# Kernel tuning notes

Hardware: AMD Instinct MI355X
Metric: run time of the kernel (lower is better)

The kernel has to match this reference:

```python
import jax, jax.numpy as jnp
import numpy as np

N_FEATURE = 12
SIGMA = 0.015
NODES = jnp.linspace(0.0, 0.3, 12)  # RBF centers, matches torch.linspace(0,0.3,12)

B, N, K, FIN = 16, 4096, 32, 4


def setup_inputs() -> dict:
    key = jax.random.key(0)
    ks = jax.random.split(key, 24)

    def make_d(ki, kd):
        idx = jax.random.randint(ki, (B, N, K), 0, N).astype(jnp.float32)
        dist = jax.random.uniform(kd, (B, N, K), minval=0.0, maxval=0.3)
        return jnp.stack([idx, dist], axis=-1)  # [B,N,K,2]

    def lin(kw, kb, fin, fout):
        W = jax.random.normal(kw, (fin, fout), jnp.float32) * (1.0 / np.sqrt(fin))
        b = jax.random.normal(kb, (fout,), jnp.float32) * 0.01
        return W, b

    x = jax.random.normal(ks[0], (B, N, FIN), jnp.float32)
    d1 = make_d(ks[1], ks[2])
    d0 = make_d(ks[3], ks[4])
    dm1 = make_d(ks[5], ks[6])
    mask = jnp.ones((B, N), dtype=bool)

    We, be = lin(ks[7], ks[8], FIN, N_FEATURE)
    Wm1, bm1 = lin(ks[9], ks[10], N_FEATURE + 12, N_FEATURE)
    Wu1, bu1 = lin(ks[11], ks[12], 2 * N_FEATURE, N_FEATURE)
    Wm0, bm0 = lin(ks[13], ks[14], N_FEATURE + 12, N_FEATURE)
    Wu0, bu0 = lin(ks[15], ks[16], 2 * N_FEATURE, N_FEATURE)
    Wmm1, bmm1 = lin(ks[17], ks[18], N_FEATURE + 12, N_FEATURE)
    Wum1, bum1 = lin(ks[19], ks[20], 2 * N_FEATURE, N_FEATURE)

    return {"x": x, "d1": d1, "d0": d0, "dm1": dm1, "mask": mask,
            "We": We, "be": be, "Wm1": Wm1, "bm1": bm1, "Wu1": Wu1, "bu1": bu1,
            "Wm0": Wm0, "bm0": bm0, "Wu0": Wu0, "bu0": bu0,
            "Wmm1": Wmm1, "bmm1": bmm1, "Wum1": Wum1, "bum1": bum1}


def _branch(h, d, Wm, bm, Wu, bu):
    # d: [B,N,K,2] -> channel 0 neighbor index, channel 1 distance
    idx = d[..., 0].astype(jnp.int32)                     # [B,N,K]
    rbf = jnp.exp(-((d[..., 1][..., None] - NODES) ** 2) / (2.0 * SIGMA ** 2))  # [B,N,K,12]
    hj = jax.vmap(lambda hb, ib: hb[ib])(h, idx)          # gather: [B,N,K,F]
    hd = jnp.concatenate([hj, rbf], axis=-1)              # [B,N,K,F+12]
    m = jax.nn.relu(hd @ Wm + bm).sum(axis=2)             # [B,N,F]
    return jax.nn.sigmoid(jnp.concatenate([h, m], axis=-1) @ Wu + bu)  # [B,N,F]


def reference(x, d1, d0, dm1, mask,
              We, be, Wm1, bm1, Wu1, bu1,
              Wm0, bm0, Wu0, bu0,
              Wmm1, bmm1, Wum1, bum1):
    h = jax.nn.relu(x @ We + be)                          # [B,N,12]
    h1 = _branch(h, d1, Wm1, bm1, Wu1, bu1)
    h0 = _branch(h, d0, Wm0, bm0, Wu0, bu0)
    hm1 = _branch(h, dm1, Wmm1, bmm1, Wum1, bum1)
    return (h1, h0, hm1)
```

## Files before the change

kernel.cpp:

```cpp
#include <hip/hip_runtime.h>
#include <hip/hip_fp16.h>
#include <math.h>

#define BBAT 16
#define NNODE 4096
#define KNB 32
#define NF 12
#define TBL 512
#define TMAIN 1024
#define NPB 256

#define LDS_BYTES 122880

__device__ __forceinline__ __half2 u2h(unsigned int u) { __half2 h; __builtin_memcpy(&h, &u, 4); return h; }
__device__ __forceinline__ unsigned int h2u(__half2 h) { unsigned int u; __builtin_memcpy(&u, &h, 4); return u; }

__device__ __forceinline__ void phi_entry(int e, const float* __restrict__ Wm, float* ph)
{
    float dd = (float)e * (0.3f / (float)TBL);
    float rbf[12];
#pragma unroll
    for (int j = 0; j < 12; j++) {
        float t = dd - (0.3f / 11.0f) * (float)j;
        rbf[j] = expf(-2222.2222222222f * t * t);
    }
#pragma unroll
    for (int c = 0; c < NF; c++) {
        float s = 0.0f;
#pragma unroll
        for (int j = 0; j < 12; j++) s = fmaf(rbf[j], Wm[(12 + j) * NF + c], s);
        ph[c] = s;
    }
}

__global__ __launch_bounds__(256) void prep_kernel(
    const float* __restrict__ x, const float* __restrict__ We, const float* __restrict__ be,
    const float* __restrict__ Wm1, const float* __restrict__ bm1,
    const float* __restrict__ Wm0, const float* __restrict__ bm0,
    const float* __restrict__ Wmm1, const float* __restrict__ bmm1,
    uint2* __restrict__ gS0, uint2* __restrict__ gS1, uint2* __restrict__ gS2,
    uint2* __restrict__ T01, uint2* __restrict__ T23, uint2* __restrict__ T45,
    uint2* __restrict__ D01, uint2* __restrict__ D23, uint2* __restrict__ D45)
{
    const int node = blockIdx.x * 256 + threadIdx.x;
    float4 xv = ((const float4*)x)[node];
    float hv[NF];
#pragma unroll
    for (int f = 0; f < NF; f++) {
        float s = be[f];
        s = fmaf(xv.x, We[0 * NF + f], s);
        s = fmaf(xv.y, We[1 * NF + f], s);
        s = fmaf(xv.z, We[2 * NF + f], s);
        s = fmaf(xv.w, We[3 * NF + f], s);
        hv[f] = fmaxf(s, 0.0f);
    }

#define DO_G(BR, WM, BM) {                                                     \
        float g[NF];                                                           \
        _Pragma("unroll") for (int c = 0; c < NF; c++) {                       \
            float s = BM[c];                                                   \
            _Pragma("unroll") for (int j = 0; j < NF; j++)                     \
                s = fmaf(hv[j], WM[j * NF + c], s);                            \
            g[c] = s;                                                          \
        }                                                                      \
        const size_t o = (size_t)(BR) * 65536 + node;                          \
        gS0[o] = make_uint2(h2u(__floats2half2_rn(g[0], g[1])),                \
                            h2u(__floats2half2_rn(g[2], g[3])));               \
        gS1[o] = make_uint2(h2u(__floats2half2_rn(g[4], g[5])),                \
                            h2u(__floats2half2_rn(g[6], g[7])));               \
        gS2[o] = make_uint2(h2u(__floats2half2_rn(g[8], g[9])),                \
                            h2u(__floats2half2_rn(g[10], g[11])));             \
    }
    DO_G(0, Wm1, bm1)
    DO_G(1, Wm0, bm0)
    DO_G(2, Wmm1, bmm1)
#undef DO_G

    if (blockIdx.x < 3) {
        const int br = blockIdx.x;
        const float* Wm = (br == 0) ? Wm1 : (br == 1) ? Wm0 : Wmm1;
        for (int i = threadIdx.x; i < TBL; i += 256) {
            float p0[NF], p1[NF];
            phi_entry(i, Wm, p0);
            phi_entry(i + 1, Wm, p1);
            __half2 w0 = __floats2half2_rn(p0[0],  p0[1]);
            __half2 w1 = __floats2half2_rn(p0[2],  p0[3]);
            __half2 w2 = __floats2half2_rn(p0[4],  p0[5]);
            __half2 w3 = __floats2half2_rn(p0[6],  p0[7]);
            __half2 w4 = __floats2half2_rn(p0[8],  p0[9]);
            __half2 w5 = __floats2half2_rn(p0[10], p0[11]);
            __half2 v0 = __floats2half2_rn(p1[0],  p1[1]);
            __half2 v1 = __floats2half2_rn(p1[2],  p1[3]);
            __half2 v2 = __floats2half2_rn(p1[4],  p1[5]);
            __half2 v3 = __floats2half2_rn(p1[6],  p1[7]);
            __half2 v4 = __floats2half2_rn(p1[8],  p1[9]);
            __half2 v5 = __floats2half2_rn(p1[10], p1[11]);
            const int o = br * TBL + i;
            T01[o] = make_uint2(h2u(w0), h2u(w1));
            T23[o] = make_uint2(h2u(w2), h2u(w3));
            T45[o] = make_uint2(h2u(w4), h2u(w5));
            D01[o] = make_uint2(h2u(__hsub2(v0, w0)), h2u(__hsub2(v1, w1)));
            D23[o] = make_uint2(h2u(__hsub2(v2, w2)), h2u(__hsub2(v3, w3)));
            D45[o] = make_uint2(h2u(__hsub2(v4, w4)), h2u(__hsub2(v5, w5)));
        }
    }
}

__global__ __launch_bounds__(TMAIN) void main_kernel(
    const float* __restrict__ x, const float* __restrict__ We, const float* __restrict__ be,
    const uint2* __restrict__ gS0, const uint2* __restrict__ gS1, const uint2* __restrict__ gS2,
    const uint2* __restrict__ T01, const uint2* __restrict__ T23, const uint2* __restrict__ T45,
    const uint2* __restrict__ D01, const uint2* __restrict__ D23, const uint2* __restrict__ D45,
    const float* __restrict__ d1, const float* __restrict__ d0, const float* __restrict__ dm1,
    const float* __restrict__ Wu1, const float* __restrict__ bu1,
    const float* __restrict__ Wu0, const float* __restrict__ bu0,
    const float* __restrict__ Wum1, const float* __restrict__ bum1,
    float* __restrict__ out)
{
    extern __shared__ char smem[];
    uint2* G0l  = (uint2*)smem;
    uint2* G1l  = (uint2*)(smem + 32768);
    uint2* G2l  = (uint2*)(smem + 65536);
    uint2* T01l = (uint2*)(smem + 98304);
    uint2* T23l = (uint2*)(smem + 102400);
    uint2* T45l = (uint2*)(smem + 106496);
    uint2* D01l = (uint2*)(smem + 110592);
    uint2* D23l = (uint2*)(smem + 114688);
    uint2* D45l = (uint2*)(smem + 118784);

    const int w = blockIdx.x;
    const int xcd = w & 7;
    const int k = w >> 3;
    const int slice = xcd + 8 * (k >> 4);
    const int chunk = k & 15;
    const int br = slice / BBAT;
    const int b  = slice % BBAT;

    const int tid = threadIdx.x;
    const int nl = tid >> 2, sub = tid & 3;
    const int n = chunk * NPB + nl;

    const float* dsel = (br == 0) ? d1 : (br == 1) ? d0 : dm1;

    const float4* dp = (const float4*)(dsel + ((size_t)b * NNODE + n) * (size_t)(KNB * 2)) + sub * 4;
    float4 dr0 = dp[0], dr1 = dp[1], dr2 = dp[2], dr3 = dp[3];

    {
        const uint4* s0 = (const uint4*)(gS0 + (size_t)slice * NNODE);
        const uint4* s1 = (const uint4*)(gS1 + (size_t)slice * NNODE);
        const uint4* s2 = (const uint4*)(gS2 + (size_t)slice * NNODE);
        uint4* L0 = (uint4*)G0l; uint4* L1 = (uint4*)G1l; uint4* L2 = (uint4*)G2l;
#pragma unroll
        for (int it = 0; it < 2; it++) {
            const int i = it * TMAIN + tid;
            L0[i] = s0[i];
            L1[i] = s1[i];
            L2[i] = s2[i];
        }
        if (tid < TBL) {
            const int o = br * TBL + tid;
            T01l[tid] = T01[o];
            T23l[tid] = T23[o];
            T45l[tid] = T45[o];
            D01l[tid] = D01[o];
            D23l[tid] = D23[o];
            D45l[tid] = D45[o];
        }
    }
    __syncthreads();

    int   jv[8];
    float uv[8];
    jv[0] = (int)dr0.x; uv[0] = dr0.y * ((float)TBL / 0.3f);
    jv[1] = (int)dr0.z; uv[1] = dr0.w * ((float)TBL / 0.3f);
    jv[2] = (int)dr1.x; uv[2] = dr1.y * ((float)TBL / 0.3f);
    jv[3] = (int)dr1.z; uv[3] = dr1.w * ((float)TBL / 0.3f);
    jv[4] = (int)dr2.x; uv[4] = dr2.y * ((float)TBL / 0.3f);
    jv[5] = (int)dr2.z; uv[5] = dr2.w * ((float)TBL / 0.3f);
    jv[6] = (int)dr3.x; uv[6] = dr3.y * ((float)TBL / 0.3f);
    jv[7] = (int)dr3.z; uv[7] = dr3.w * ((float)TBL / 0.3f);

    float m[NF];
#pragma unroll
    for (int f = 0; f < NF; f++) m[f] = 0.0f;

#define ACC(O, G, T0, DT) {                                                    \
        __half2 phi = __hfma2(f2, u2h(DT), u2h(T0));                           \
        __half2 s2 = __hadd2(u2h(G), phi);                                     \
        float2 sf = __half22float2(s2);                                        \
        m[O]     += fmaxf(sf.x, 0.0f);                                         \
        m[O + 1] += fmaxf(sf.y, 0.0f);                                         \
    }

#define EDGE(GC0, GC1, GC2, GN0, GN1, GN2, E, PREF)                            \
    {                                                                          \
        if (PREF) { int jn = jv[(E) + 1];                                      \
            GN0 = G0l[jn]; GN1 = G1l[jn]; GN2 = G2l[jn]; }                     \
        float uu = uv[E];                                                      \
        int ii = (int)uu;                                                      \
        ii = min(ii, TBL - 1);                                                 \
        float fr = uu - (float)ii;                                             \
        __half2 f2 = __float2half2_rn(fr);                                     \
        uint2 ta = T01l[ii], tb = T23l[ii], tc = T45l[ii];                     \
        uint2 da = D01l[ii], db = D23l[ii], dc = D45l[ii];                     \
        ACC(0,  GC0.x, ta.x, da.x)                                             \
        ACC(2,  GC0.y, ta.y, da.y)                                             \
        ACC(4,  GC1.x, tb.x, db.x)                                             \
        ACC(6,  GC1.y, tb.y, db.y)                                             \
        ACC(8,  GC2.x, tc.x, dc.x)                                             \
        ACC(10, GC2.y, tc.y, dc.y)                                             \
    }

    uint2 pa0, pa1, pa2, pb0, pb1, pb2;
    { int j0 = jv[0]; pa0 = G0l[j0]; pa1 = G1l[j0]; pa2 = G2l[j0]; }
    EDGE(pa0, pa1, pa2, pb0, pb1, pb2, 0, 1)
    EDGE(pb0, pb1, pb2, pa0, pa1, pa2, 1, 1)
    EDGE(pa0, pa1, pa2, pb0, pb1, pb2, 2, 1)
    EDGE(pb0, pb1, pb2, pa0, pa1, pa2, 3, 1)
    EDGE(pa0, pa1, pa2, pb0, pb1, pb2, 4, 1)
    EDGE(pb0, pb1, pb2, pa0, pa1, pa2, 5, 1)
    EDGE(pa0, pa1, pa2, pb0, pb1, pb2, 6, 1)
    EDGE(pb0, pb1, pb2, pa0, pa1, pa2, 7, 0)

#undef EDGE
#undef ACC

#pragma unroll
    for (int f = 0; f < NF; f++) m[f] += __shfl_xor(m[f], 1);
#pragma unroll
    for (int f = 0; f < NF; f++) m[f] += __shfl_xor(m[f], 2);

    const float* Wu = (br == 0) ? Wu1 : (br == 1) ? Wu0 : Wum1;
    const float* bu = (br == 0) ? bu1 : (br == 1) ? bu0 : bum1;

    float4 xv = ((const float4*)x)[(size_t)b * NNODE + n];
    float hv[NF];
#pragma unroll
    for (int f = 0; f < NF; f++) {
        float s = be[f];
        s = fmaf(xv.x, We[0 * NF + f], s);
        s = fmaf(xv.y, We[1 * NF + f], s);
        s = fmaf(xv.z, We[2 * NF + f], s);
        s = fmaf(xv.w, We[3 * NF + f], s);
        hv[f] = fmaxf(s, 0.0f);
    }

    const int f0 = sub * 3;
    float* op = out + ((size_t)slice * NNODE + n) * NF + f0;
#pragma unroll
    for (int ff = 0; ff < 3; ff++) {
        const int f = f0 + ff;
        float a = bu[f];
#pragma unroll
        for (int j = 0; j < NF; j++) a = fmaf(hv[j], Wu[j * NF + f], a);
#pragma unroll
        for (int j = 0; j < NF; j++) a = fmaf(m[j], Wu[(NF + j) * NF + f], a);
        op[ff] = 1.0f / (1.0f + __expf(-a));
    }
}

extern "C" void kernel_launch(void* const* d_in, const int* in_sizes, int n_in,
                              void* d_out, int out_size, void* d_ws, size_t ws_size,
                              hipStream_t stream)
{
    const float* x    = (const float*)d_in[0];
    const float* d1   = (const float*)d_in[1];
    const float* d0   = (const float*)d_in[2];
    const float* dm1  = (const float*)d_in[3];
    const float* We   = (const float*)d_in[5];
    const float* be   = (const float*)d_in[6];
    const float* Wm1  = (const float*)d_in[7];
    const float* bm1  = (const float*)d_in[8];
    const float* Wu1  = (const float*)d_in[9];
    const float* bu1  = (const float*)d_in[10];
    const float* Wm0  = (const float*)d_in[11];
    const float* bm0  = (const float*)d_in[12];
    const float* Wu0  = (const float*)d_in[13];
    const float* bu0  = (const float*)d_in[14];
    const float* Wmm1 = (const float*)d_in[15];
    const float* bmm1 = (const float*)d_in[16];
    const float* Wum1 = (const float*)d_in[17];
    const float* bum1 = (const float*)d_in[18];

    char* ws = (char*)d_ws;
    uint2* gS0 = (uint2*)ws;
    uint2* gS1 = (uint2*)(ws + 1572864);
    uint2* gS2 = (uint2*)(ws + 3145728);
    uint2* T01 = (uint2*)(ws + 4718592);
    uint2* T23 = (uint2*)(ws + 4730880);
    uint2* T45 = (uint2*)(ws + 4743168);
    uint2* D01 = (uint2*)(ws + 4755456);
    uint2* D23 = (uint2*)(ws + 4767744);
    uint2* D45 = (uint2*)(ws + 4780032);

    hipFuncSetAttribute((const void*)main_kernel,
                        hipFuncAttributeMaxDynamicSharedMemorySize, LDS_BYTES);

    prep_kernel<<<dim3(256), 256, 0, stream>>>(
        x, We, be, Wm1, bm1, Wm0, bm0, Wmm1, bmm1,
        gS0, gS1, gS2, T01, T23, T45, D01, D23, D45);
    main_kernel<<<dim3(768), TMAIN, LDS_BYTES, stream>>>(
        x, We, be, gS0, gS1, gS2, T01, T23, T45, D01, D23, D45,
        d1, d0, dm1, Wu1, bu1, Wu0, bu0, Wum1, bum1, (float*)d_out);
}
```

Before: 152.5 us.

## Pack gather and table arrays into wider LDS records and batch edge loads

```diff
diff --git a/kernel.cpp b/kernel.cpp
--- a/kernel.cpp
+++ b/kernel.cpp
@@ -38,9 +38,8 @@
     const float* __restrict__ Wm1, const float* __restrict__ bm1,
     const float* __restrict__ Wm0, const float* __restrict__ bm0,
     const float* __restrict__ Wmm1, const float* __restrict__ bmm1,
-    uint2* __restrict__ gS0, uint2* __restrict__ gS1, uint2* __restrict__ gS2,
-    uint2* __restrict__ T01, uint2* __restrict__ T23, uint2* __restrict__ T45,
-    uint2* __restrict__ D01, uint2* __restrict__ D23, uint2* __restrict__ D45)
+    uint4* __restrict__ gA, uint2* __restrict__ gB,
+    uint4* __restrict__ TA, uint4* __restrict__ TB, uint4* __restrict__ TC)
 {
     const int node = blockIdx.x * 256 + threadIdx.x;
     float4 xv = ((const float4*)x)[node];
@@ -64,12 +63,12 @@
             g[c] = s;                                                          \
         }                                                                      \
         const size_t o = (size_t)(BR) * 65536 + node;                          \
-        gS0[o] = make_uint2(h2u(__floats2half2_rn(g[0], g[1])),                \
-                            h2u(__floats2half2_rn(g[2], g[3])));               \
-        gS1[o] = make_uint2(h2u(__floats2half2_rn(g[4], g[5])),                \
-                            h2u(__floats2half2_rn(g[6], g[7])));               \
-        gS2[o] = make_uint2(h2u(__floats2half2_rn(g[8], g[9])),                \
-                            h2u(__floats2half2_rn(g[10], g[11])));             \
+        gA[o] = make_uint4(h2u(__floats2half2_rn(g[0], g[1])),                 \
+                           h2u(__floats2half2_rn(g[2], g[3])),                 \
+                           h2u(__floats2half2_rn(g[4], g[5])),                 \
+                           h2u(__floats2half2_rn(g[6], g[7])));                \
+        gB[o] = make_uint2(h2u(__floats2half2_rn(g[8], g[9])),                 \
+                           h2u(__floats2half2_rn(g[10], g[11])));              \
     }
     DO_G(0, Wm1, bm1)
     DO_G(1, Wm0, bm0)
@@ -96,21 +95,17 @@
             __half2 v4 = __floats2half2_rn(p1[8],  p1[9]);
             __half2 v5 = __floats2half2_rn(p1[10], p1[11]);
             const int o = br * TBL + i;
-            T01[o] = make_uint2(h2u(w0), h2u(w1));
-            T23[o] = make_uint2(h2u(w2), h2u(w3));
-            T45[o] = make_uint2(h2u(w4), h2u(w5));
-            D01[o] = make_uint2(h2u(__hsub2(v0, w0)), h2u(__hsub2(v1, w1)));
-            D23[o] = make_uint2(h2u(__hsub2(v2, w2)), h2u(__hsub2(v3, w3)));
-            D45[o] = make_uint2(h2u(__hsub2(v4, w4)), h2u(__hsub2(v5, w5)));
+            TA[o] = make_uint4(h2u(w0), h2u(w1), h2u(__hsub2(v0, w0)), h2u(__hsub2(v1, w1)));
+            TB[o] = make_uint4(h2u(w2), h2u(w3), h2u(__hsub2(v2, w2)), h2u(__hsub2(v3, w3)));
+            TC[o] = make_uint4(h2u(w4), h2u(w5), h2u(__hsub2(v4, w4)), h2u(__hsub2(v5, w5)));
         }
     }
 }
 
-__global__ __launch_bounds__(TMAIN) void main_kernel(
+__global__ __launch_bounds__(TMAIN, 4) void main_kernel(
     const float* __restrict__ x, const float* __restrict__ We, const float* __restrict__ be,
-    const uint2* __restrict__ gS0, const uint2* __restrict__ gS1, const uint2* __restrict__ gS2,
-    const uint2* __restrict__ T01, const uint2* __restrict__ T23, const uint2* __restrict__ T45,
-    const uint2* __restrict__ D01, const uint2* __restrict__ D23, const uint2* __restrict__ D45,
+    const uint4* __restrict__ gA, const uint2* __restrict__ gB,
+    const uint4* __restrict__ TA, const uint4* __restrict__ TB, const uint4* __restrict__ TC,
     const float* __restrict__ d1, const float* __restrict__ d0, const float* __restrict__ dm1,
     const float* __restrict__ Wu1, const float* __restrict__ bu1,
     const float* __restrict__ Wu0, const float* __restrict__ bu0,
@@ -118,15 +113,11 @@
     float* __restrict__ out)
 {
     extern __shared__ char smem[];
-    uint2* G0l  = (uint2*)smem;
-    uint2* G1l  = (uint2*)(smem + 32768);
-    uint2* G2l  = (uint2*)(smem + 65536);
-    uint2* T01l = (uint2*)(smem + 98304);
-    uint2* T23l = (uint2*)(smem + 102400);
-    uint2* T45l = (uint2*)(smem + 106496);
-    uint2* D01l = (uint2*)(smem + 110592);
-    uint2* D23l = (uint2*)(smem + 114688);
-    uint2* D45l = (uint2*)(smem + 118784);
+    uint4* GAl = (uint4*)smem;
+    uint2* GBl = (uint2*)(smem + 65536);
+    uint4* TAl = (uint4*)(smem + 98304);
+    uint4* TBl = (uint4*)(smem + 106496);
+    uint4* TCl = (uint4*)(smem + 114688);
 
     const int w = blockIdx.x;
     const int xcd = w & 7;
@@ -146,39 +137,42 @@
     float4 dr0 = dp[0], dr1 = dp[1], dr2 = dp[2], dr3 = dp[3];
 
     {
-        const uint4* s0 = (const uint4*)(gS0 + (size_t)slice * NNODE);
-        const uint4* s1 = (const uint4*)(gS1 + (size_t)slice * NNODE);
-        const uint4* s2 = (const uint4*)(gS2 + (size_t)slice * NNODE);
-        uint4* L0 = (uint4*)G0l; uint4* L1 = (uint4*)G1l; uint4* L2 = (uint4*)G2l;
-#pragma unroll
-        for (int it = 0; it < 2; it++) {
-            const int i = it * TMAIN + tid;
-            L0[i] = s0[i];
-            L1[i] = s1[i];
-            L2[i] = s2[i];
-        }
+        const uint4* sA = gA + (size_t)slice * NNODE;
+        const uint4* sB = (const uint4*)(gB + (size_t)slice * NNODE);
+        uint4* LB = (uint4*)GBl;
+#pragma unroll
+        for (int it = 0; it < 4; it++) GAl[it * TMAIN + tid] = sA[it * TMAIN + tid];
+#pragma unroll
+        for (int it = 0; it < 2; it++) LB[it * TMAIN + tid] = sB[it * TMAIN + tid];
         if (tid < TBL) {
             const int o = br * TBL + tid;
-            T01l[tid] = T01[o];
-            T23l[tid] = T23[o];
-            T45l[tid] = T45[o];
-            D01l[tid] = D01[o];
-            D23l[tid] = D23[o];
-            D45l[tid] = D45[o];
+            TAl[tid] = TA[o];
+            TBl[tid] = TB[o];
+            TCl[tid] = TC[o];
         }
     }
     __syncthreads();
 
-    int   jv[8];
-    float uv[8];
-    jv[0] = (int)dr0.x; uv[0] = dr0.y * ((float)TBL / 0.3f);
-    jv[1] = (int)dr0.z; uv[1] = dr0.w * ((float)TBL / 0.3f);
-    jv[2] = (int)dr1.x; uv[2] = dr1.y * ((float)TBL / 0.3f);
-    jv[3] = (int)dr1.z; uv[3] = dr1.w * ((float)TBL / 0.3f);
-    jv[4] = (int)dr2.x; uv[4] = dr2.y * ((float)TBL / 0.3f);
-    jv[5] = (int)dr2.z; uv[5] = dr2.w * ((float)TBL / 0.3f);
-    jv[6] = (int)dr3.x; uv[6] = dr3.y * ((float)TBL / 0.3f);
-    jv[7] = (int)dr3.z; uv[7] = dr3.w * ((float)TBL / 0.3f);
+    int   jv[8], iv[8];
+    float fv[8];
+    {
+        float uvv[8];
+        jv[0] = (int)dr0.x; uvv[0] = dr0.y * ((float)TBL / 0.3f);
+        jv[1] = (int)dr0.z; uvv[1] = dr0.w * ((float)TBL / 0.3f);
+        jv[2] = (int)dr1.x; uvv[2] = dr1.y * ((float)TBL / 0.3f);
+        jv[3] = (int)dr1.z; uvv[3] = dr1.w * ((float)TBL / 0.3f);
+        jv[4] = (int)dr2.x; uvv[4] = dr2.y * ((float)TBL / 0.3f);
+        jv[5] = (int)dr2.z; uvv[5] = dr2.w * ((float)TBL / 0.3f);
+        jv[6] = (int)dr3.x; uvv[6] = dr3.y * ((float)TBL / 0.3f);
+        jv[7] = (int)dr3.z; uvv[7] = dr3.w * ((float)TBL / 0.3f);
+#pragma unroll
+        for (int r = 0; r < 8; r++) {
+            int ii = (int)uvv[r];
+            ii = min(ii, TBL - 1);
+            iv[r] = ii;
+            fv[r] = uvv[r] - (float)ii;
+        }
+    }
 
     float m[NF];
 #pragma unroll
@@ -192,37 +186,46 @@
         m[O + 1] += fmaxf(sf.y, 0.0f);                                         \
     }
 
-#define EDGE(GC0, GC1, GC2, GN0, GN1, GN2, E, PREF)                            \
-    {                                                                          \
-        if (PREF) { int jn = jv[(E) + 1];                                      \
-            GN0 = G0l[jn]; GN1 = G1l[jn]; GN2 = G2l[jn]; }                     \
-        float uu = uv[E];                                                      \
-        int ii = (int)uu;                                                      \
-        ii = min(ii, TBL - 1);                                                 \
-        float fr = uu - (float)ii;                                             \
-        __half2 f2 = __float2half2_rn(fr);                                     \
-        uint2 ta = T01l[ii], tb = T23l[ii], tc = T45l[ii];                     \
-        uint2 da = D01l[ii], db = D23l[ii], dc = D45l[ii];                     \
-        ACC(0,  GC0.x, ta.x, da.x)                                             \
-        ACC(2,  GC0.y, ta.y, da.y)                                             \
-        ACC(4,  GC1.x, tb.x, db.x)                                             \
-        ACC(6,  GC1.y, tb.y, db.y)                                             \
-        ACC(8,  GC2.x, tc.x, dc.x)                                             \
-        ACC(10, GC2.y, tc.y, dc.y)                                             \
-    }
-
-    uint2 pa0, pa1, pa2, pb0, pb1, pb2;
-    { int j0 = jv[0]; pa0 = G0l[j0]; pa1 = G1l[j0]; pa2 = G2l[j0]; }
-    EDGE(pa0, pa1, pa2, pb0, pb1, pb2, 0, 1)
-    EDGE(pb0, pb1, pb2, pa0, pa1, pa2, 1, 1)
-    EDGE(pa0, pa1, pa2, pb0, pb1, pb2, 2, 1)
-    EDGE(pb0, pb1, pb2, pa0, pa1, pa2, 3, 1)
-    EDGE(pa0, pa1, pa2, pb0, pb1, pb2, 4, 1)
-    EDGE(pb0, pb1, pb2, pa0, pa1, pa2, 5, 1)
-    EDGE(pa0, pa1, pa2, pb0, pb1, pb2, 6, 1)
-    EDGE(pb0, pb1, pb2, pa0, pa1, pa2, 7, 0)
-
-#undef EDGE
+#define ISSUE(P, E) {                                                          \
+        int j0 = jv[E], j1 = jv[(E) + 1];                                      \
+        P##ga0 = GAl[j0]; P##gb0 = GBl[j0];                                    \
+        P##ga1 = GAl[j1]; P##gb1 = GBl[j1];                                    \
+        int i0 = iv[E], i1 = iv[(E) + 1];                                      \
+        P##ta0 = TAl[i0]; P##tb0 = TBl[i0]; P##tc0 = TCl[i0];                  \
+        P##ta1 = TAl[i1]; P##tb1 = TBl[i1]; P##tc1 = TCl[i1];                  \
+    }
+
+#define PROC1(GA, GB, TT, TU, TV, E) {                                         \
+        __half2 f2 = __float2half2_rn(fv[E]);                                  \
+        ACC(0,  GA.x, TT.x, TT.z)                                              \
+        ACC(2,  GA.y, TT.y, TT.w)                                              \
+        ACC(4,  GA.z, TU.x, TU.z)                                              \
+        ACC(6,  GA.w, TU.y, TU.w)                                              \
+        ACC(8,  GB.x, TV.x, TV.z)                                              \
+        ACC(10, GB.y, TV.y, TV.w)                                              \
+    }
+
+#define PROC(P, E)                                                             \
+        PROC1(P##ga0, P##gb0, P##ta0, P##tb0, P##tc0, E)                       \
+        PROC1(P##ga1, P##gb1, P##ta1, P##tb1, P##tc1, (E) + 1)
+
+    uint4 Aga0, Aga1, Ata0, Atb0, Atc0, Ata1, Atb1, Atc1;
+    uint2 Agb0, Agb1;
+    uint4 Bga0, Bga1, Bta0, Btb0, Btc0, Bta1, Btb1, Btc1;
+    uint2 Bgb0, Bgb1;
+
+    ISSUE(A, 0)
+    ISSUE(B, 2)
+    PROC(A, 0)
+    ISSUE(A, 4)
+    PROC(B, 2)
+    ISSUE(B, 6)
+    PROC(A, 4)
+    PROC(B, 6)
+
+#undef PROC
+#undef PROC1
+#undef ISSUE
 #undef ACC
 
 #pragma unroll
@@ -283,23 +286,18 @@
     const float* bum1 = (const float*)d_in[18];
 
     char* ws = (char*)d_ws;
-    uint2* gS0 = (uint2*)ws;
-    uint2* gS1 = (uint2*)(ws + 1572864);
-    uint2* gS2 = (uint2*)(ws + 3145728);
-    uint2* T01 = (uint2*)(ws + 4718592);
-    uint2* T23 = (uint2*)(ws + 4730880);
-    uint2* T45 = (uint2*)(ws + 4743168);
-    uint2* D01 = (uint2*)(ws + 4755456);
-    uint2* D23 = (uint2*)(ws + 4767744);
-    uint2* D45 = (uint2*)(ws + 4780032);
+    uint4* gA = (uint4*)ws;
+    uint2* gB = (uint2*)(ws + 3145728);
+    uint4* TA = (uint4*)(ws + 4718592);
+    uint4* TB = (uint4*)(ws + 4743168);
+    uint4* TC = (uint4*)(ws + 4767744);
 
     hipFuncSetAttribute((const void*)main_kernel,
                         hipFuncAttributeMaxDynamicSharedMemorySize, LDS_BYTES);
 
     prep_kernel<<<dim3(256), 256, 0, stream>>>(
-        x, We, be, Wm1, bm1, Wm0, bm0, Wmm1, bmm1,
-        gS0, gS1, gS2, T01, T23, T45, D01, D23, D45);
+        x, We, be, Wm1, bm1, Wm0, bm0, Wmm1, bmm1, gA, gB, TA, TB, TC);
     main_kernel<<<dim3(768), TMAIN, LDS_BYTES, stream>>>(
-        x, We, be, gS0, gS1, gS2, T01, T23, T45, D01, D23, D45,
+        x, We, be, gA, gB, TA, TB, TC,
         d1, d0, dm1, Wu1, bu1, Wu0, bu0, Wum1, bum1, (float*)d_out);
 }
```

Result: no change. 150.1 us (-1.6%).
